# Kernel optimization log

Hardware: AMD Instinct MI355X
Metric: run time of the kernel (lower is better)

## Reference

```python
import jax, jax.numpy as jnp
import numpy as np

V, D, B, L = 433, 120, 4096, 16  # vocab, d_model, batch, seq_len
H4 = 4 * D
LN_EPS = 1e-5


def setup_inputs() -> dict:
    key = jax.random.key(0)
    ks = jax.random.split(key, 12)
    s = 1.0 / np.sqrt(D)  # PyTorch LSTM init range
    u = lambda k, shape: jax.random.uniform(k, shape, jnp.float32, -s, s)
    return {
        "x": jax.random.randint(ks[0], (B, L), 0, V, dtype=jnp.int32),
        "embed": jax.random.normal(ks[1], (V, D), jnp.float32) * 0.02,
        "Wih0": u(ks[2], (H4, D)), "Whh0": u(ks[3], (H4, D)),
        "bih0": u(ks[4], (H4,)), "bhh0": u(ks[5], (H4,)),
        "Wih1": u(ks[6], (H4, D)), "Whh1": u(ks[7], (H4, D)),
        "bih1": u(ks[8], (H4,)), "bhh1": u(ks[9], (H4,)),
        "gamma": jnp.ones((D,), jnp.float32),
        "beta": jnp.zeros((D,), jnp.float32),
    }


def _lstm_layer(x, Wih, Whh, bih, bhh):
    """One LSTM layer, batch_first input [B,L,D] -> [B,L,H]. PyTorch gate order i,f,g,o."""
    b, _, _ = x.shape
    h_dim = Whh.shape[1]
    # Precompute input contribution for all timesteps in one big GEMM.
    xg = jnp.einsum('bld,gd->blg', x, Wih) + bih + bhh  # [B,L,4H]

    def step(carry, g_t):
        h, c = carry
        gates = g_t + h @ Whh.T  # [B,4H]
        i, f, g, o = jnp.split(gates, 4, axis=-1)
        c = jax.nn.sigmoid(f) * c + jax.nn.sigmoid(i) * jnp.tanh(g)
        h = jax.nn.sigmoid(o) * jnp.tanh(c)
        return (h, c), h

    init = (jnp.zeros((b, h_dim), x.dtype), jnp.zeros((b, h_dim), x.dtype))
    _, hs = jax.lax.scan(step, init, jnp.swapaxes(xg, 0, 1))  # [L,B,H]
    return jnp.swapaxes(hs, 0, 1)


def _layernorm(h, gamma, beta):
    mu = jnp.mean(h, axis=-1, keepdims=True)
    var = jnp.mean(jnp.square(h - mu), axis=-1, keepdims=True)
    return (h - mu) / jnp.sqrt(var + LN_EPS) * gamma + beta


def reference(x, embed, Wih0, Whh0, bih0, bhh0, Wih1, Whh1, bih1, bhh1, gamma, beta):
    h = embed[x]                               # [B,L,D] token embedding
    h = _lstm_layer(h, Wih0, Whh0, bih0, bhh0)  # layer 0
    h = _lstm_layer(h, Wih1, Whh1, bih1, bhh1)  # layer 1
    out = _layernorm(h, gamma, beta)
    logits = jnp.einsum('bld,vd->blv', out, embed)  # tied-embedding head (no bias)
    return logits
```

## Files before the change

### kernel.cpp

```cpp
#include <hip/hip_runtime.h>


#define VSZ 433
#define DIM 120
#define BSZ 4096
#define SEQ 16
#define H4  480
#define KP  128
#define NPAD 448
#define NT_HEAD (NPAD/16)
#define TB  16
#define GP  484
#define HP  136

typedef unsigned int   u32;
typedef unsigned short u16;
typedef __attribute__((ext_vector_type(8))) short    v8bf;
typedef __attribute__((ext_vector_type(8))) _Float16 v8h;
typedef __attribute__((ext_vector_type(4))) float    v4f;

__device__ __forceinline__ u16 f2bf(float f){
  union{float f;u32 u;}z; z.f=f;
  u32 u = z.u + 0x7fffu + ((z.u>>16)&1u);
  return (u16)(u>>16);
}
__device__ __forceinline__ u32 packh2(float a, float b){
  union{_Float16 h[2]; u32 u;} z;
  z.h[0] = (_Float16)a; z.h[1] = (_Float16)b;
  return z.u;
}

#define EW_OFF   0u
#define B1S_OFF  831488u
#define EMBP_OFF 833408u
#define HB0_OFF  948096u

#define PREP_BLKS 113

__global__ __launch_bounds__(512) void k_init(const float* __restrict__ embed,
                                              const float* __restrict__ Wih0,
                                              const float* __restrict__ bih0,
                                              const float* __restrict__ bhh0,
                                              const float* __restrict__ bih1,
                                              const float* __restrict__ bhh1,
                                              float* __restrict__ EW,
                                              u16* __restrict__ embP,
                                              float* __restrict__ b1s)
{
  __shared__ float e[DIM];
  const int tid = threadIdx.x;
  if (blockIdx.x < VSZ) {
    const int v = blockIdx.x;
    if (tid < DIM) e[tid] = embed[v*DIM + tid];
    __syncthreads();
    if (tid < H4) {
      float acc = bih0[tid] + bhh0[tid];
      #pragma unroll
      for (int k0 = 0; k0 < DIM; k0 += 4) {
        float4 w = *(const float4*)(Wih0 + tid*DIM + k0);
        acc = fmaf(e[k0+0], w.x, acc);
        acc = fmaf(e[k0+1], w.y, acc);
        acc = fmaf(e[k0+2], w.z, acc);
        acc = fmaf(e[k0+3], w.w, acc);
      }
      EW[v*H4 + tid] = acc;
    }
  } else {
    const int idx = (blockIdx.x - VSZ)*512 + tid;
    if (idx < NPAD*KP) {
      int n = idx >> 7, k = idx & 127;
      embP[idx] = (n < VSZ && k < DIM) ? f2bf(embed[n*DIM + k]) : (u16)0;
    } else if (idx < NPAD*KP + H4) {
      int g = idx - NPAD*KP;
      b1s[g] = bih1[g] + bhh1[g];
    }
  }
}

__global__ __launch_bounds__(512) void k_rec(const float* __restrict__ Whh0,
                                             const float* __restrict__ EW,
                                             const int* __restrict__ x,
                                             const float* __restrict__ Wih1,
                                             const float* __restrict__ Whh1,
                                             const float* __restrict__ b1s,
                                             const float* __restrict__ gamma,
                                             const float* __restrict__ beta,
                                             const u16* __restrict__ embP,
                                             _Float16* __restrict__ hb0,
                                             float* __restrict__ out)
{
  __shared__ float gLs[TB][GP];
  __shared__ __align__(16) _Float16 hLh[TB][HP];
  __shared__ __align__(16) u16 hnL[TB][HP];
  __shared__ __align__(16) u16 embL[NPAD][HP];
  __shared__ int xL[TB*SEQ];

  const int tid  = threadIdx.x;
  const int wave = tid >> 6, lane = tid & 63;
  const int cl   = lane & 15, quad = lane >> 4;
  const int b0   = blockIdx.x * TB;

  for (int i = tid; i < TB*SEQ; i += 512) xL[i] = x[b0*SEQ + i];
  for (int i = tid; i < TB*HP; i += 512) (&hLh[0][0])[i] = (_Float16)0.f;
  for (int c = tid; c < NPAD*16; c += 512) {
    const int rw = c >> 4, c16 = c & 15;
    *(v8bf*)&embL[rw][c16*8] = *(const v8bf*)&embP[(size_t)rw*KP + c16*8];
  }
  __syncthreads();

  const int prow = wave*2;
  const bool act = lane < 60;
  const int d0   = lane*2;

  {
    v8h Bf[4][4];
    #pragma unroll
    for (int i = 0; i < 4; ++i) {
      const int nt = wave*4 + i;
      const bool vld = (nt < 30);
      const int n = vld ? nt*16 + cl : 0;
      #pragma unroll
      for (int kt = 0; kt < 4; ++kt) {
        const int k0 = kt*32 + quad*8;
        v8h f = {0,0,0,0,0,0,0,0};
        if (vld && k0 < DIM) {
          float4 q0 = *(const float4*)(Whh0 + n*DIM + k0);
          float4 q1 = *(const float4*)(Whh0 + n*DIM + k0 + 4);
          f[0]=(_Float16)q0.x; f[1]=(_Float16)q0.y; f[2]=(_Float16)q0.z; f[3]=(_Float16)q0.w;
          f[4]=(_Float16)q1.x; f[5]=(_Float16)q1.y; f[6]=(_Float16)q1.z; f[7]=(_Float16)q1.w;
        }
        Bf[i][kt] = f;
      }
    }

    float srcv[4][4];
    auto load_src = [&](int t) {
      #pragma unroll
      for (int i = 0; i < 4; ++i) {
        const int nt = wave*4 + i;
        if (nt < 30) {
          const int n = nt*16 + cl;
          #pragma unroll
          for (int r = 0; r < 4; ++r)
            srcv[i][r] = EW[(size_t)xL[(quad*4 + r)*SEQ + t]*H4 + n];
        }
      }
    };
    load_src(0);

    float C0[2][2] = {{0.f,0.f},{0.f,0.f}};

    for (int t = 0; t < SEQ; ++t) {
      __syncthreads();
      v8h Af[4];
      #pragma unroll
      for (int kt = 0; kt < 4; ++kt)
        Af[kt] = *(const v8h*)&hLh[cl][kt*32 + quad*8];
      v4f acc[4];
      #pragma unroll
      for (int i = 0; i < 4; ++i) {
        acc[i][0]=srcv[i][0]; acc[i][1]=srcv[i][1];
        acc[i][2]=srcv[i][2]; acc[i][3]=srcv[i][3];
      }
      #pragma unroll
      for (int i = 0; i < 4; ++i)
        if (wave*4 + i < 30) {
          #pragma unroll
          for (int kt = 0; kt < 4; ++kt)
            acc[i] = __builtin_amdgcn_mfma_f32_16x16x32_f16(Af[kt], Bf[i][kt], acc[i], 0, 0, 0);
        }
      if (t + 1 < SEQ) load_src(t + 1);
      #pragma unroll
      for (int i = 0; i < 4; ++i) {
        const int nt = wave*4 + i;
        if (nt < 30) {
          #pragma unroll
          for (int r = 0; r < 4; ++r)
            gLs[quad*4 + r][nt*16 + cl] = acc[i][r];
        }
      }
      __syncthreads();
      #pragma unroll
      for (int rr = 0; rr < 2; ++rr) {
        const int row = prow + rr;
        if (act) {
          const float2 gi = *(const float2*)&gLs[row][d0      ];
          const float2 gf = *(const float2*)&gLs[row][d0 + 120];
          const float2 gg = *(const float2*)&gLs[row][d0 + 240];
          const float2 go = *(const float2*)&gLs[row][d0 + 360];
          float h2[2];
          #pragma unroll
          for (int k = 0; k < 2; ++k) {
            const float vi = k ? gi.y : gi.x, vf = k ? gf.y : gf.x;
            const float vg = k ? gg.y : gg.x, vo = k ? go.y : go.x;
            const float si = 1.f / (1.f + __expf(-vi));
            const float sf = 1.f / (1.f + __expf(-vf));
            const float tg = 1.f - 2.f / (__expf(2.f*vg) + 1.f);
            const float so = 1.f / (1.f + __expf(-vo));
            const float c  = sf * C0[rr][k] + si * tg;
            C0[rr][k] = c;
            const float tc = 1.f - 2.f / (__expf(2.f*c) + 1.f);
            h2[k] = so * tc;
          }
          *(u32*)&hLh[row][d0] = packh2(h2[0], h2[1]);
          *(u32*)&hb0[((size_t)t*BSZ + b0 + row)*KP + d0] = packh2(h2[0], h2[1]);
        } else {
          *(u32*)&hb0[((size_t)t*BSZ + b0 + row)*KP + 120 + 2*(lane - 60)] = 0u;
        }
      }
    }
  }

  __syncthreads();

  const float* Wih1p = Wih1;
  const float* Whh1p = Whh1;
  const float* b1sp  = b1s;
  asm volatile("" : "+s"(Wih1p), "+s"(Whh1p), "+s"(b1sp) :: "memory");

  for (int i = tid; i < TB*HP; i += 512) (&hLh[0][0])[i] = (_Float16)0.f;

  v8h Bi[4][4], Bh[4][4];
  float bias[4];
  #pragma unroll
  for (int i = 0; i < 4; ++i) {
    const int nt = wave*4 + i;
    const bool vld = (nt < 30);
    const int n = vld ? nt*16 + cl : 0;
    bias[i] = vld ? b1sp[n] : 0.f;
    #pragma unroll
    for (int kt = 0; kt < 4; ++kt) {
      const int k0 = kt*32 + quad*8;
      v8h fi = {0,0,0,0,0,0,0,0}, fh = {0,0,0,0,0,0,0,0};
      if (vld && k0 < DIM) {
        float4 q0 = *(const float4*)(Wih1p + n*DIM + k0);
        float4 q1 = *(const float4*)(Wih1p + n*DIM + k0 + 4);
        fi[0]=(_Float16)q0.x; fi[1]=(_Float16)q0.y; fi[2]=(_Float16)q0.z; fi[3]=(_Float16)q0.w;
        fi[4]=(_Float16)q1.x; fi[5]=(_Float16)q1.y; fi[6]=(_Float16)q1.z; fi[7]=(_Float16)q1.w;
        float4 p0 = *(const float4*)(Whh1p + n*DIM + k0);
        float4 p1 = *(const float4*)(Whh1p + n*DIM + k0 + 4);
        fh[0]=(_Float16)p0.x; fh[1]=(_Float16)p0.y; fh[2]=(_Float16)p0.z; fh[3]=(_Float16)p0.w;
        fh[4]=(_Float16)p1.x; fh[5]=(_Float16)p1.y; fh[6]=(_Float16)p1.z; fh[7]=(_Float16)p1.w;
      }
      Bi[i][kt] = fi;
      Bh[i][kt] = fh;
    }
  }

  float gmm[2] = {0.f, 0.f}, bta[2] = {0.f, 0.f};
  if (act) {
    gmm[0] = gamma[d0]; gmm[1] = gamma[d0+1];
    bta[0] = beta[d0];  bta[1] = beta[d0+1];
  }
  float C1[2][2] = {{0.f,0.f},{0.f,0.f}};

  v8h A0n[4];
  #pragma unroll
  for (int kt = 0; kt < 4; ++kt)
    A0n[kt] = *(const v8h*)&hb0[((size_t)0*BSZ + b0 + cl)*KP + kt*32 + quad*8];
  __syncthreads();

  for (int t = 0; t < SEQ; ++t) {
    v8h A0c[4], A1[4];
    #pragma unroll
    for (int kt = 0; kt < 4; ++kt) A0c[kt] = A0n[kt];
    #pragma unroll
    for (int kt = 0; kt < 4; ++kt)
      A1[kt] = *(const v8h*)&hLh[cl][kt*32 + quad*8];
    if (t + 1 < SEQ) {
      #pragma unroll
      for (int kt = 0; kt < 4; ++kt)
        A0n[kt] = *(const v8h*)&hb0[((size_t)(t+1)*BSZ + b0 + cl)*KP + kt*32 + quad*8];
    }
    v4f acc[4];
    #pragma unroll
    for (int i = 0; i < 4; ++i)
      acc[i] = (v4f){bias[i], bias[i], bias[i], bias[i]};
    #pragma unroll
    for (int i = 0; i < 4; ++i)
      if (wave*4 + i < 30) {
        #pragma unroll
        for (int kt = 0; kt < 4; ++kt) {
          acc[i] = __builtin_amdgcn_mfma_f32_16x16x32_f16(A0c[kt], Bi[i][kt], acc[i], 0, 0, 0);
          acc[i] = __builtin_amdgcn_mfma_f32_16x16x32_f16(A1[kt],  Bh[i][kt], acc[i], 0, 0, 0);
        }
      }
    #pragma unroll
    for (int i = 0; i < 4; ++i) {
      const int nt = wave*4 + i;
      if (nt < 30) {
        #pragma unroll
        for (int r = 0; r < 4; ++r)
          gLs[quad*4 + r][nt*16 + cl] = acc[i][r];
      }
    }
    __syncthreads();
    float h2[2][2] = {{0.f,0.f},{0.f,0.f}};
    float s1[2] = {0.f, 0.f}, s2[2] = {0.f, 0.f};
    #pragma unroll
    for (int rr = 0; rr < 2; ++rr) {
      const int row = prow + rr;
      if (act) {
        const float2 gi = *(const float2*)&gLs[row][d0      ];
        const float2 gf = *(const float2*)&gLs[row][d0 + 120];
        const float2 gg = *(const float2*)&gLs[row][d0 + 240];
        const float2 go = *(const float2*)&gLs[row][d0 + 360];
        #pragma unroll
        for (int k = 0; k < 2; ++k) {
          const float vi = k ? gi.y : gi.x, vf = k ? gf.y : gf.x;
          const float vg = k ? gg.y : gg.x, vo = k ? go.y : go.x;
          const float si = 1.f / (1.f + __expf(-vi));
          const float sf = 1.f / (1.f + __expf(-vf));
          const float tg = 1.f - 2.f / (__expf(2.f*vg) + 1.f);
          const float so = 1.f / (1.f + __expf(-vo));
          const float c  = sf * C1[rr][k] + si * tg;
          C1[rr][k] = c;
          const float tc = 1.f - 2.f / (__expf(2.f*c) + 1.f);
          const float h  = so * tc;
          h2[rr][k] = h;
          s1[rr] += h;
          s2[rr] = fmaf(h, h, s2[rr]);
        }
        *(u32*)&hLh[row][d0] = packh2(h2[rr][0], h2[rr][1]);
      }
    }
    #pragma unroll
    for (int m = 32; m >= 1; m >>= 1) {
      s1[0] += __shfl_xor(s1[0], m);
      s2[0] += __shfl_xor(s2[0], m);
      s1[1] += __shfl_xor(s1[1], m);
      s2[1] += __shfl_xor(s2[1], m);
    }
    #pragma unroll
    for (int rr = 0; rr < 2; ++rr) {
      const int row = prow + rr;
      const float mu = s1[rr] * (1.f/DIM);
      const float var = s2[rr] * (1.f/DIM) - mu*mu;
      const float rs = rsqrtf(var + 1e-5f);
      if (act) {
        const float v0 = fmaf((h2[rr][0] - mu)*rs, gmm[0], bta[0]);
        const float v1 = fmaf((h2[rr][1] - mu)*rs, gmm[1], bta[1]);
        *(u32*)&hnL[row][d0] = (u32)f2bf(v0) | ((u32)f2bf(v1) << 16);
      } else {
        *(u32*)&hnL[row][120 + 2*(lane - 60)] = 0u;
      }
    }
    __syncthreads();

    {
      v8bf a[4];
      #pragma unroll
      for (int kt = 0; kt < 4; ++kt)
        a[kt] = *(const v8bf*)&hnL[cl][kt*32 + quad*8];
      #pragma unroll
      for (int j = 0; j < 4; ++j) {
        const int nt = wave + 8*j;
        if (nt < NT_HEAD) {
          const int n = nt*16 + cl;
          v8bf bfr[4];
          #pragma unroll
          for (int kt = 0; kt < 4; ++kt)
            bfr[kt] = *(const v8bf*)&embL[n][kt*32 + quad*8];
          v4f hacc = {0.f, 0.f, 0.f, 0.f};
          #pragma unroll
          for (int kt = 0; kt < 4; ++kt)
            hacc = __builtin_amdgcn_mfma_f32_16x16x32_bf16(a[kt], bfr[kt], hacc, 0, 0, 0);
          if (n < VSZ) {
            #pragma unroll
            for (int r = 0; r < 4; ++r)
              out[((size_t)(b0 + quad*4 + r)*SEQ + t)*VSZ + n] = hacc[r];
          }
        }
      }
    }
  }
}

extern "C" void kernel_launch(void* const* d_in, const int* in_sizes, int n_in,
                              void* d_out, int out_size, void* d_ws, size_t ws_size,
                              hipStream_t stream)
{
  (void)in_sizes; (void)n_in; (void)out_size; (void)ws_size;
  const int*   x     = (const int*)d_in[0];
  const float* embed = (const float*)d_in[1];
  const float* Wih0  = (const float*)d_in[2];
  const float* Whh0  = (const float*)d_in[3];
  const float* bih0  = (const float*)d_in[4];
  const float* bhh0  = (const float*)d_in[5];
  const float* Wih1  = (const float*)d_in[6];
  const float* Whh1  = (const float*)d_in[7];
  const float* bih1  = (const float*)d_in[8];
  const float* bhh1  = (const float*)d_in[9];
  const float* gamma = (const float*)d_in[10];
  const float* beta  = (const float*)d_in[11];

  char* ws = (char*)d_ws;
  float*     EW   = (float*)(ws + EW_OFF);
  float*     b1s  = (float*)(ws + B1S_OFF);
  u16*       embP = (u16*)(ws + EMBP_OFF);
  _Float16*  hb0  = (_Float16*)(ws + HB0_OFF);

  k_init<<<VSZ + PREP_BLKS, 512, 0, stream>>>(embed, Wih0, bih0, bhh0, bih1, bhh1,
                                              EW, embP, b1s);
  k_rec <<<BSZ/TB, 512, 0, stream>>>(Whh0, EW, x, Wih1, Whh1, b1s, gamma, beta,
                                     embP, hb0, (float*)d_out);
}
```

Measured before the change: 257.2 us.

## Interleave gate columns per wave, keep layer-0 states in LDS, pipeline head behind LSTM

Gate rows are permuted so that each wave's MFMA output tile holds the i,f,g,o values for its own hidden units. The cell update then reads from a per-wave scratch with only a wave barrier, which removes one block-wide barrier per step and the shared gate buffer. Layer-0 hidden states stay in LDS instead of round-tripping through global memory. The embedding head reads a pre-swizzled fragment layout straight from global memory instead of staging into LDS. Layer-1 recurrence, the LayerNorm reduction via a partial-sum buffer, and the head GEMM are software-pipelined across steps with double buffers. The cost is larger LDS use from the sixteen-step hb0 buffer and the head B operand coming through cache rather than LDS.

```diff
diff --git a/kernel.cpp b/kernel.cpp
--- a/kernel.cpp
+++ b/kernel.cpp
@@ -8,10 +8,10 @@
 #define H4  480
 #define KP  128
 #define NPAD 448
-#define NT_HEAD (NPAD/16)
+#define NT_HEAD 28
 #define TB  16
-#define GP  484
 #define HP  136
+#define SCRW 68
 
 typedef unsigned int   u32;
 typedef unsigned short u16;
@@ -30,12 +30,12 @@
   return z.u;
 }
 
-#define EW_OFF   0u
-#define B1S_OFF  831488u
-#define EMBP_OFF 833408u
-#define HB0_OFF  948096u
-
-#define PREP_BLKS 113
+#define EW_OFF    0u
+#define B1S_OFF   831488u
+#define EMBF_OFF  833408u
+
+#define PREP_N    (NPAD*KP + H4)
+#define PREP_BLKS ((PREP_N + 511)/512)
 
 __global__ __launch_bounds__(512) void k_init(const float* __restrict__ embed,
                                               const float* __restrict__ Wih0,
@@ -44,7 +44,7 @@
                                               const float* __restrict__ bih1,
                                               const float* __restrict__ bhh1,
                                               float* __restrict__ EW,
-                                              u16* __restrict__ embP,
+                                              u16* __restrict__ embF,
                                               float* __restrict__ b1s)
 {
   __shared__ float e[DIM];
@@ -69,8 +69,10 @@
     const int idx = (blockIdx.x - VSZ)*512 + tid;
     if (idx < NPAD*KP) {
       int n = idx >> 7, k = idx & 127;
-      embP[idx] = (n < VSZ && k < DIM) ? f2bf(embed[n*DIM + k]) : (u16)0;
-    } else if (idx < NPAD*KP + H4) {
+      int nt = n >> 4, cl = n & 15, kt = k >> 5, quad = (k >> 3) & 3, j = k & 7;
+      int fidx = ((((nt*4 + kt)*4 + quad)*16 + cl) << 3) + j;
+      embF[fidx] = (n < VSZ && k < DIM) ? f2bf(embed[n*DIM + k]) : (u16)0;
+    } else if (idx < PREP_N) {
       int g = idx - NPAD*KP;
       b1s[g] = bih1[g] + bhh1[g];
     }
@@ -85,160 +87,145 @@
                                              const float* __restrict__ b1s,
                                              const float* __restrict__ gamma,
                                              const float* __restrict__ beta,
-                                             const u16* __restrict__ embP,
-                                             _Float16* __restrict__ hb0,
+                                             const u16* __restrict__ embF,
                                              float* __restrict__ out)
 {
-  __shared__ float gLs[TB][GP];
-  __shared__ __align__(16) _Float16 hLh[TB][HP];
-  __shared__ __align__(16) u16 hnL[TB][HP];
-  __shared__ __align__(16) u16 embL[NPAD][HP];
+  __shared__ float scr[8][TB][SCRW];
+  __shared__ __align__(16) _Float16 hLh0[2][TB][HP];
+  __shared__ __align__(16) _Float16 hLh1[2][TB][HP];
+  __shared__ __align__(16) u16 hnLD[2][TB][HP];
+  __shared__ __align__(16) _Float16 hb0L[SEQ][TB][HP];
+  __shared__ float prt[2][TB][8][2];
   __shared__ int xL[TB*SEQ];
 
   const int tid  = threadIdx.x;
   const int wave = tid >> 6, lane = tid & 63;
   const int cl   = lane & 15, quad = lane >> 4;
   const int b0   = blockIdx.x * TB;
+  const int row  = lane & 15, lg = lane >> 4;
+  const int dl0  = wave*16 + lg*4;
+  const bool vdim = (dl0 < DIM);
 
   for (int i = tid; i < TB*SEQ; i += 512) xL[i] = x[b0*SEQ + i];
-  for (int i = tid; i < TB*HP; i += 512) (&hLh[0][0])[i] = (_Float16)0.f;
-  for (int c = tid; c < NPAD*16; c += 512) {
-    const int rw = c >> 4, c16 = c & 15;
-    *(v8bf*)&embL[rw][c16*8] = *(const v8bf*)&embP[(size_t)rw*KP + c16*8];
-  }
+  for (int i = tid; i < 2*TB*HP; i += 512) {
+    (&hLh0[0][0][0])[i] = (_Float16)0.f;
+    (&hLh1[0][0][0])[i] = (_Float16)0.f;
+  }
+
+  int orow[4];
+  #pragma unroll
+  for (int i = 0; i < 4; ++i) {
+    const int p = (wave*4 + i)*16 + cl;
+    orow[i] = (p & 3)*120 + (p >> 2);
+  }
+
+  v8h Bf0[4][4];
+  #pragma unroll
+  for (int i = 0; i < 4; ++i) {
+    const bool vld = (wave*4 + i < 30);
+    #pragma unroll
+    for (int kt = 0; kt < 4; ++kt) {
+      const int k0 = kt*32 + quad*8;
+      v8h f = {0,0,0,0,0,0,0,0};
+      if (vld && k0 < DIM) {
+        float4 q0 = *(const float4*)(Whh0 + orow[i]*DIM + k0);
+        float4 q1 = *(const float4*)(Whh0 + orow[i]*DIM + k0 + 4);
+        f[0]=(_Float16)q0.x; f[1]=(_Float16)q0.y; f[2]=(_Float16)q0.z; f[3]=(_Float16)q0.w;
+        f[4]=(_Float16)q1.x; f[5]=(_Float16)q1.y; f[6]=(_Float16)q1.z; f[7]=(_Float16)q1.w;
+      }
+      Bf0[i][kt] = f;
+    }
+  }
+
+  float srcv[4][4] = {{0.f,0.f,0.f,0.f},{0.f,0.f,0.f,0.f},
+                      {0.f,0.f,0.f,0.f},{0.f,0.f,0.f,0.f}};
+  auto load_src = [&](int t) {
+    #pragma unroll
+    for (int i = 0; i < 4; ++i) {
+      if (wave*4 + i < 30) {
+        #pragma unroll
+        for (int r = 0; r < 4; ++r)
+          srcv[i][r] = EW[(size_t)xL[(quad*4 + r)*SEQ + t]*H4 + orow[i]];
+      }
+    }
+  };
   __syncthreads();
-
-  const int prow = wave*2;
-  const bool act = lane < 60;
-  const int d0   = lane*2;
-
-  {
-    v8h Bf[4][4];
+  load_src(0);
+
+  float C0[4] = {0.f, 0.f, 0.f, 0.f};
+
+  for (int t = 0; t < SEQ; ++t) {
+    v8h Af[4];
+    #pragma unroll
+    for (int kt = 0; kt < 4; ++kt)
+      Af[kt] = *(const v8h*)&hLh0[t & 1][cl][kt*32 + quad*8];
+    v4f acc[4];
     #pragma unroll
     for (int i = 0; i < 4; ++i) {
-      const int nt = wave*4 + i;
-      const bool vld = (nt < 30);
-      const int n = vld ? nt*16 + cl : 0;
-      #pragma unroll
-      for (int kt = 0; kt < 4; ++kt) {
-        const int k0 = kt*32 + quad*8;
-        v8h f = {0,0,0,0,0,0,0,0};
-        if (vld && k0 < DIM) {
-          float4 q0 = *(const float4*)(Whh0 + n*DIM + k0);
-          float4 q1 = *(const float4*)(Whh0 + n*DIM + k0 + 4);
-          f[0]=(_Float16)q0.x; f[1]=(_Float16)q0.y; f[2]=(_Float16)q0.z; f[3]=(_Float16)q0.w;
-          f[4]=(_Float16)q1.x; f[5]=(_Float16)q1.y; f[6]=(_Float16)q1.z; f[7]=(_Float16)q1.w;
-        }
-        Bf[i][kt] = f;
-      }
-    }
-
-    float srcv[4][4];
-    auto load_src = [&](int t) {
-      #pragma unroll
-      for (int i = 0; i < 4; ++i) {
-        const int nt = wave*4 + i;
-        if (nt < 30) {
-          const int n = nt*16 + cl;
-          #pragma unroll
-          for (int r = 0; r < 4; ++r)
-            srcv[i][r] = EW[(size_t)xL[(quad*4 + r)*SEQ + t]*H4 + n];
-        }
-      }
-    };
-    load_src(0);
-
-    float C0[2][2] = {{0.f,0.f},{0.f,0.f}};
-
-    for (int t = 0; t < SEQ; ++t) {
-      __syncthreads();
-      v8h Af[4];
-      #pragma unroll
-      for (int kt = 0; kt < 4; ++kt)
-        Af[kt] = *(const v8h*)&hLh[cl][kt*32 + quad*8];
-      v4f acc[4];
-      #pragma unroll
-      for (int i = 0; i < 4; ++i) {
-        acc[i][0]=srcv[i][0]; acc[i][1]=srcv[i][1];
-        acc[i][2]=srcv[i][2]; acc[i][3]=srcv[i][3];
-      }
+      acc[i][0]=srcv[i][0]; acc[i][1]=srcv[i][1];
+      acc[i][2]=srcv[i][2]; acc[i][3]=srcv[i][3];
+    }
+    #pragma unroll
+    for (int kt = 0; kt < 4; ++kt)
       #pragma unroll
       for (int i = 0; i < 4; ++i)
-        if (wave*4 + i < 30) {
-          #pragma unroll
-          for (int kt = 0; kt < 4; ++kt)
-            acc[i] = __builtin_amdgcn_mfma_f32_16x16x32_f16(Af[kt], Bf[i][kt], acc[i], 0, 0, 0);
-        }
-      if (t + 1 < SEQ) load_src(t + 1);
-      #pragma unroll
-      for (int i = 0; i < 4; ++i) {
-        const int nt = wave*4 + i;
-        if (nt < 30) {
-          #pragma unroll
-          for (int r = 0; r < 4; ++r)
-            gLs[quad*4 + r][nt*16 + cl] = acc[i][r];
-        }
-      }
-      __syncthreads();
-      #pragma unroll
-      for (int rr = 0; rr < 2; ++rr) {
-        const int row = prow + rr;
-        if (act) {
-          const float2 gi = *(const float2*)&gLs[row][d0      ];
-          const float2 gf = *(const float2*)&gLs[row][d0 + 120];
-          const float2 gg = *(const float2*)&gLs[row][d0 + 240];
-          const float2 go = *(const float2*)&gLs[row][d0 + 360];
-          float h2[2];
-          #pragma unroll
-          for (int k = 0; k < 2; ++k) {
-            const float vi = k ? gi.y : gi.x, vf = k ? gf.y : gf.x;
-            const float vg = k ? gg.y : gg.x, vo = k ? go.y : go.x;
-            const float si = 1.f / (1.f + __expf(-vi));
-            const float sf = 1.f / (1.f + __expf(-vf));
-            const float tg = 1.f - 2.f / (__expf(2.f*vg) + 1.f);
-            const float so = 1.f / (1.f + __expf(-vo));
-            const float c  = sf * C0[rr][k] + si * tg;
-            C0[rr][k] = c;
-            const float tc = 1.f - 2.f / (__expf(2.f*c) + 1.f);
-            h2[k] = so * tc;
-          }
-          *(u32*)&hLh[row][d0] = packh2(h2[0], h2[1]);
-          *(u32*)&hb0[((size_t)t*BSZ + b0 + row)*KP + d0] = packh2(h2[0], h2[1]);
-        } else {
-          *(u32*)&hb0[((size_t)t*BSZ + b0 + row)*KP + 120 + 2*(lane - 60)] = 0u;
-        }
-      }
-    }
-  }
-
-  __syncthreads();
+        if (wave*4 + i < 30)
+          acc[i] = __builtin_amdgcn_mfma_f32_16x16x32_f16(Af[kt], Bf0[i][kt], acc[i], 0, 0, 0);
+    if (t + 1 < SEQ) load_src(t + 1);
+    #pragma unroll
+    for (int i = 0; i < 4; ++i)
+      if (wave*4 + i < 30) {
+        #pragma unroll
+        for (int r = 0; r < 4; ++r)
+          scr[wave][quad*4 + r][16*i + cl] = acc[i][r];
+      }
+    __builtin_amdgcn_wave_barrier();
+    asm volatile("s_waitcnt lgkmcnt(0)" ::: "memory");
+    __builtin_amdgcn_sched_barrier(0);
+    float h0v[4];
+    #pragma unroll
+    for (int j = 0; j < 4; ++j) {
+      const float4 gq = *(const float4*)&scr[wave][row][16*lg + 4*j];
+      const float si = 1.f / (1.f + __expf(-gq.x));
+      const float sf = 1.f / (1.f + __expf(-gq.y));
+      const float tg = 1.f - 2.f / (__expf(2.f*gq.z) + 1.f);
+      const float so = 1.f / (1.f + __expf(-gq.w));
+      const float c  = sf * C0[j] + si * tg;
+      C0[j] = c;
+      const float tc = 1.f - 2.f / (__expf(2.f*c) + 1.f);
+      h0v[j] = so * tc;
+    }
+    uint2 pk; pk.x = 0u; pk.y = 0u;
+    if (vdim) { pk.x = packh2(h0v[0], h0v[1]); pk.y = packh2(h0v[2], h0v[3]); }
+    *(uint2*)&hLh0[(t+1) & 1][row][dl0] = pk;
+    *(uint2*)&hb0L[t][row][dl0] = pk;
+    __syncthreads();
+  }
 
   const float* Wih1p = Wih1;
   const float* Whh1p = Whh1;
   const float* b1sp  = b1s;
-  asm volatile("" : "+s"(Wih1p), "+s"(Whh1p), "+s"(b1sp) :: "memory");
-
-  for (int i = tid; i < TB*HP; i += 512) (&hLh[0][0])[i] = (_Float16)0.f;
+  const float* gmp   = gamma;
+  const float* btp   = beta;
+  asm volatile("" : "+s"(Wih1p), "+s"(Whh1p), "+s"(b1sp), "+s"(gmp), "+s"(btp) :: "memory");
 
   v8h Bi[4][4], Bh[4][4];
   float bias[4];
   #pragma unroll
   for (int i = 0; i < 4; ++i) {
-    const int nt = wave*4 + i;
-    const bool vld = (nt < 30);
-    const int n = vld ? nt*16 + cl : 0;
-    bias[i] = vld ? b1sp[n] : 0.f;
+    const bool vld = (wave*4 + i < 30);
+    bias[i] = vld ? b1sp[orow[i]] : 0.f;
     #pragma unroll
     for (int kt = 0; kt < 4; ++kt) {
       const int k0 = kt*32 + quad*8;
       v8h fi = {0,0,0,0,0,0,0,0}, fh = {0,0,0,0,0,0,0,0};
       if (vld && k0 < DIM) {
-        float4 q0 = *(const float4*)(Wih1p + n*DIM + k0);
-        float4 q1 = *(const float4*)(Wih1p + n*DIM + k0 + 4);
+        float4 q0 = *(const float4*)(Wih1p + orow[i]*DIM + k0);
+        float4 q1 = *(const float4*)(Wih1p + orow[i]*DIM + k0 + 4);
         fi[0]=(_Float16)q0.x; fi[1]=(_Float16)q0.y; fi[2]=(_Float16)q0.z; fi[3]=(_Float16)q0.w;
         fi[4]=(_Float16)q1.x; fi[5]=(_Float16)q1.y; fi[6]=(_Float16)q1.z; fi[7]=(_Float16)q1.w;
-        float4 p0 = *(const float4*)(Whh1p + n*DIM + k0);
-        float4 p1 = *(const float4*)(Whh1p + n*DIM + k0 + 4);
+        float4 p0 = *(const float4*)(Whh1p + orow[i]*DIM + k0);
+        float4 p1 = *(const float4*)(Whh1p + orow[i]*DIM + k0 + 4);
         fh[0]=(_Float16)p0.x; fh[1]=(_Float16)p0.y; fh[2]=(_Float16)p0.z; fh[3]=(_Float16)p0.w;
         fh[4]=(_Float16)p1.x; fh[5]=(_Float16)p1.y; fh[6]=(_Float16)p1.z; fh[7]=(_Float16)p1.w;
       }
@@ -246,125 +233,56 @@
       Bh[i][kt] = fh;
     }
   }
-
-  float gmm[2] = {0.f, 0.f}, bta[2] = {0.f, 0.f};
-  if (act) {
-    gmm[0] = gamma[d0]; gmm[1] = gamma[d0+1];
-    bta[0] = beta[d0];  bta[1] = beta[d0+1];
-  }
-  float C1[2][2] = {{0.f,0.f},{0.f,0.f}};
-
-  v8h A0n[4];
-  #pragma unroll
-  for (int kt = 0; kt < 4; ++kt)
-    A0n[kt] = *(const v8h*)&hb0[((size_t)0*BSZ + b0 + cl)*KP + kt*32 + quad*8];
-  __syncthreads();
-
-  for (int t = 0; t < SEQ; ++t) {
-    v8h A0c[4], A1[4];
-    #pragma unroll
-    for (int kt = 0; kt < 4; ++kt) A0c[kt] = A0n[kt];
-    #pragma unroll
-    for (int kt = 0; kt < 4; ++kt)
-      A1[kt] = *(const v8h*)&hLh[cl][kt*32 + quad*8];
-    if (t + 1 < SEQ) {
+  float gmm4[4] = {0.f,0.f,0.f,0.f}, bta4[4] = {0.f,0.f,0.f,0.f};
+  if (vdim) {
+    #pragma unroll
+    for (int j = 0; j < 4; ++j) { gmm4[j] = gmp[dl0+j]; bta4[j] = btp[dl0+j]; }
+  }
+  float C1[4] = {0.f,0.f,0.f,0.f};
+  float h1prev[4] = {0.f,0.f,0.f,0.f};
+
+  for (int s = 0; s <= SEQ + 1; ++s) {
+    if (s >= 1 && s <= SEQ) {
+      const float* pr = &prt[(s-1) & 1][row][0][0];
+      const float4 q0 = *(const float4*)(pr);
+      const float4 q1 = *(const float4*)(pr + 4);
+      const float4 q2 = *(const float4*)(pr + 8);
+      const float4 q3 = *(const float4*)(pr + 12);
+      const float s1 = q0.x+q0.z + q1.x+q1.z + q2.x+q2.z + q3.x+q3.z;
+      const float s2 = q0.y+q0.w + q1.y+q1.w + q2.y+q2.w + q3.y+q3.w;
+      const float mu = s1 * (1.f/DIM);
+      const float var = s2 * (1.f/DIM) - mu*mu;
+      const float rs = rsqrtf(var + 1e-5f);
+      uint2 pk; pk.x = 0u; pk.y = 0u;
+      if (vdim) {
+        const float v0 = fmaf((h1prev[0]-mu)*rs, gmm4[0], bta4[0]);
+        const float v1 = fmaf((h1prev[1]-mu)*rs, gmm4[1], bta4[1]);
+        const float v2 = fmaf((h1prev[2]-mu)*rs, gmm4[2], bta4[2]);
+        const float v3 = fmaf((h1prev[3]-mu)*rs, gmm4[3], bta4[3]);
+        pk.x = (u32)f2bf(v0) | ((u32)f2bf(v1) << 16);
+        pk.y = (u32)f2bf(v2) | ((u32)f2bf(v3) << 16);
+      }
+      *(uint2*)&hnLD[(s-1) & 1][row][dl0] = pk;
+    }
+    if (s >= 2) {
+      const int t = s - 2;
+      v8bf a[4];
       #pragma unroll
       for (int kt = 0; kt < 4; ++kt)
-        A0n[kt] = *(const v8h*)&hb0[((size_t)(t+1)*BSZ + b0 + cl)*KP + kt*32 + quad*8];
-    }
-    v4f acc[4];
-    #pragma unroll
-    for (int i = 0; i < 4; ++i)
-      acc[i] = (v4f){bias[i], bias[i], bias[i], bias[i]};
-    #pragma unroll
-    for (int i = 0; i < 4; ++i)
-      if (wave*4 + i < 30) {
-        #pragma unroll
-        for (int kt = 0; kt < 4; ++kt) {
-          acc[i] = __builtin_amdgcn_mfma_f32_16x16x32_f16(A0c[kt], Bi[i][kt], acc[i], 0, 0, 0);
-          acc[i] = __builtin_amdgcn_mfma_f32_16x16x32_f16(A1[kt],  Bh[i][kt], acc[i], 0, 0, 0);
-        }
-      }
-    #pragma unroll
-    for (int i = 0; i < 4; ++i) {
-      const int nt = wave*4 + i;
-      if (nt < 30) {
-        #pragma unroll
-        for (int r = 0; r < 4; ++r)
-          gLs[quad*4 + r][nt*16 + cl] = acc[i][r];
-      }
-    }
-    __syncthreads();
-    float h2[2][2] = {{0.f,0.f},{0.f,0.f}};
-    float s1[2] = {0.f, 0.f}, s2[2] = {0.f, 0.f};
-    #pragma unroll
-    for (int rr = 0; rr < 2; ++rr) {
-      const int row = prow + rr;
-      if (act) {
-        const float2 gi = *(const float2*)&gLs[row][d0      ];
-        const float2 gf = *(const float2*)&gLs[row][d0 + 120];
-        const float2 gg = *(const float2*)&gLs[row][d0 + 240];
-        const float2 go = *(const float2*)&gLs[row][d0 + 360];
-        #pragma unroll
-        for (int k = 0; k < 2; ++k) {
-          const float vi = k ? gi.y : gi.x, vf = k ? gf.y : gf.x;
-          const float vg = k ? gg.y : gg.x, vo = k ? go.y : go.x;
-          const float si = 1.f / (1.f + __expf(-vi));
-          const float sf = 1.f / (1.f + __expf(-vf));
-          const float tg = 1.f - 2.f / (__expf(2.f*vg) + 1.f);
-          const float so = 1.f / (1.f + __expf(-vo));
-          const float c  = sf * C1[rr][k] + si * tg;
-          C1[rr][k] = c;
-          const float tc = 1.f - 2.f / (__expf(2.f*c) + 1.f);
-          const float h  = so * tc;
-          h2[rr][k] = h;
-          s1[rr] += h;
-          s2[rr] = fmaf(h, h, s2[rr]);
-        }
-        *(u32*)&hLh[row][d0] = packh2(h2[rr][0], h2[rr][1]);
-      }
-    }
-    #pragma unroll
-    for (int m = 32; m >= 1; m >>= 1) {
-      s1[0] += __shfl_xor(s1[0], m);
-      s2[0] += __shfl_xor(s2[0], m);
-      s1[1] += __shfl_xor(s1[1], m);
-      s2[1] += __shfl_xor(s2[1], m);
-    }
-    #pragma unroll
-    for (int rr = 0; rr < 2; ++rr) {
-      const int row = prow + rr;
-      const float mu = s1[rr] * (1.f/DIM);
-      const float var = s2[rr] * (1.f/DIM) - mu*mu;
-      const float rs = rsqrtf(var + 1e-5f);
-      if (act) {
-        const float v0 = fmaf((h2[rr][0] - mu)*rs, gmm[0], bta[0]);
-        const float v1 = fmaf((h2[rr][1] - mu)*rs, gmm[1], bta[1]);
-        *(u32*)&hnL[row][d0] = (u32)f2bf(v0) | ((u32)f2bf(v1) << 16);
-      } else {
-        *(u32*)&hnL[row][120 + 2*(lane - 60)] = 0u;
-      }
-    }
-    __syncthreads();
-
-    {
-      v8bf a[4];
-      #pragma unroll
-      for (int kt = 0; kt < 4; ++kt)
-        a[kt] = *(const v8bf*)&hnL[cl][kt*32 + quad*8];
+        a[kt] = *(const v8bf*)&hnLD[(s-2) & 1][cl][kt*32 + quad*8];
       #pragma unroll
       for (int j = 0; j < 4; ++j) {
-        const int nt = wave + 8*j;
-        if (nt < NT_HEAD) {
-          const int n = nt*16 + cl;
+        const int nth = wave + 8*j;
+        if (nth < NT_HEAD) {
           v8bf bfr[4];
           #pragma unroll
           for (int kt = 0; kt < 4; ++kt)
-            bfr[kt] = *(const v8bf*)&embL[n][kt*32 + quad*8];
+            bfr[kt] = *(const v8bf*)&embF[(((size_t)nth*4 + kt)*64 + lane)*8];
           v4f hacc = {0.f, 0.f, 0.f, 0.f};
           #pragma unroll
           for (int kt = 0; kt < 4; ++kt)
             hacc = __builtin_amdgcn_mfma_f32_16x16x32_bf16(a[kt], bfr[kt], hacc, 0, 0, 0);
+          const int n = nth*16 + cl;
           if (n < VSZ) {
             #pragma unroll
             for (int r = 0; r < 4; ++r)
@@ -373,6 +291,64 @@
         }
       }
     }
+    if (s < SEQ) {
+      v8h A0[4], A1[4];
+      #pragma unroll
+      for (int kt = 0; kt < 4; ++kt) {
+        A0[kt] = *(const v8h*)&hb0L[s][cl][kt*32 + quad*8];
+        A1[kt] = *(const v8h*)&hLh1[s & 1][cl][kt*32 + quad*8];
+      }
+      v4f acc[4];
+      #pragma unroll
+      for (int i = 0; i < 4; ++i)
+        acc[i] = (v4f){bias[i], bias[i], bias[i], bias[i]};
+      #pragma unroll
+      for (int kt = 0; kt < 4; ++kt)
+        #pragma unroll
+        for (int i = 0; i < 4; ++i)
+          if (wave*4 + i < 30) {
+            acc[i] = __builtin_amdgcn_mfma_f32_16x16x32_f16(A0[kt], Bi[i][kt], acc[i], 0, 0, 0);
+            acc[i] = __builtin_amdgcn_mfma_f32_16x16x32_f16(A1[kt], Bh[i][kt], acc[i], 0, 0, 0);
+          }
+      #pragma unroll
+      for (int i = 0; i < 4; ++i)
+        if (wave*4 + i < 30) {
+          #pragma unroll
+          for (int r = 0; r < 4; ++r)
+            scr[wave][quad*4 + r][16*i + cl] = acc[i][r];
+        }
+      __builtin_amdgcn_wave_barrier();
+      asm volatile("s_waitcnt lgkmcnt(0)" ::: "memory");
+      __builtin_amdgcn_sched_barrier(0);
+      #pragma unroll
+      for (int j = 0; j < 4; ++j) {
+        const float4 gq = *(const float4*)&scr[wave][row][16*lg + 4*j];
+        const float si = 1.f / (1.f + __expf(-gq.x));
+        const float sf = 1.f / (1.f + __expf(-gq.y));
+        const float tg = 1.f - 2.f / (__expf(2.f*gq.z) + 1.f);
+        const float so = 1.f / (1.f + __expf(-gq.w));
+        const float c  = sf * C1[j] + si * tg;
+        C1[j] = c;
+        const float tc = 1.f - 2.f / (__expf(2.f*c) + 1.f);
+        h1prev[j] = so * tc;
+      }
+      uint2 pk; pk.x = 0u; pk.y = 0u;
+      if (vdim) { pk.x = packh2(h1prev[0], h1prev[1]); pk.y = packh2(h1prev[2], h1prev[3]); }
+      *(uint2*)&hLh1[(s+1) & 1][row][dl0] = pk;
+      float s1l = 0.f, s2l = 0.f;
+      if (vdim) {
+        s1l = h1prev[0] + h1prev[1] + h1prev[2] + h1prev[3];
+        s2l = h1prev[0]*h1prev[0] + h1prev[1]*h1prev[1]
+            + h1prev[2]*h1prev[2] + h1prev[3]*h1prev[3];
+      }
+      s1l += __shfl_xor(s1l, 16); s1l += __shfl_xor(s1l, 32);
+      s2l += __shfl_xor(s2l, 16); s2l += __shfl_xor(s2l, 32);
+      if (lane < 16) {
+        prt[s & 1][lane][wave][0] = s1l;
+        prt[s & 1][lane][wave][1] = s2l;
+      }
+    }
+    __syncthreads();
   }
 }
 
@@ -395,13 +371,12 @@
   const float* beta  = (const float*)d_in[11];
 
   char* ws = (char*)d_ws;
-  float*     EW   = (float*)(ws + EW_OFF);
-  float*     b1s  = (float*)(ws + B1S_OFF);
-  u16*       embP = (u16*)(ws + EMBP_OFF);
-  _Float16*  hb0  = (_Float16*)(ws + HB0_OFF);
+  float* EW   = (float*)(ws + EW_OFF);
+  float* b1s  = (float*)(ws + B1S_OFF);
+  u16*   embF = (u16*)(ws + EMBF_OFF);
 
   k_init<<<VSZ + PREP_BLKS, 512, 0, stream>>>(embed, Wih0, bih0, bhh0, bih1, bhh1,
-                                              EW, embP, b1s);
+                                              EW, embF, b1s);
   k_rec <<<BSZ/TB, 512, 0, stream>>>(Whh0, EW, x, Wih1, Whh1, b1s, gamma, beta,
-                                     embP, hb0, (float*)d_out);
-}
+                                     embF, (float*)d_out);
+}
```

Result: slower. 320.3 us (+24.5%).

## Keep layer-0 hidden states in LDS and read head weights pre-swizzled from global

Applied to the files above, without the earlier changes.

Layer-0 hidden states for all timesteps now stay in a shared-memory buffer instead of a global scratch array that layer 1 read back. The 448x136 bf16 embedding copy in LDS is removed. The head GEMM now loads its B fragments straight from a global buffer that k_init writes in MFMA fragment order, so each lane reads contiguous 16-byte chunks. NT_HEAD drops to 28, which skips the all-padding tile. Together these cut LDS use, which may allow more blocks per CU, and remove a global round trip, at the cost of head weights being read from L2/global on every timestep.

```diff
diff --git a/kernel.cpp b/kernel.cpp
--- a/kernel.cpp
+++ b/kernel.cpp
@@ -8,7 +8,7 @@
 #define H4  480
 #define KP  128
 #define NPAD 448
-#define NT_HEAD (NPAD/16)
+#define NT_HEAD 28
 #define TB  16
 #define GP  484
 #define HP  136
@@ -30,12 +30,12 @@
   return z.u;
 }
 
-#define EW_OFF   0u
-#define B1S_OFF  831488u
-#define EMBP_OFF 833408u
-#define HB0_OFF  948096u
-
-#define PREP_BLKS 113
+#define EW_OFF    0u
+#define B1S_OFF   831488u
+#define EMBF_OFF  833408u
+
+#define PREP_N    (NPAD*KP + H4)
+#define PREP_BLKS ((PREP_N + 511)/512)
 
 __global__ __launch_bounds__(512) void k_init(const float* __restrict__ embed,
                                               const float* __restrict__ Wih0,
@@ -44,7 +44,7 @@
                                               const float* __restrict__ bih1,
                                               const float* __restrict__ bhh1,
                                               float* __restrict__ EW,
-                                              u16* __restrict__ embP,
+                                              u16* __restrict__ embF,
                                               float* __restrict__ b1s)
 {
   __shared__ float e[DIM];
@@ -69,8 +69,10 @@
     const int idx = (blockIdx.x - VSZ)*512 + tid;
     if (idx < NPAD*KP) {
       int n = idx >> 7, k = idx & 127;
-      embP[idx] = (n < VSZ && k < DIM) ? f2bf(embed[n*DIM + k]) : (u16)0;
-    } else if (idx < NPAD*KP + H4) {
+      int nt = n >> 4, cl = n & 15, kt = k >> 5, quad = (k >> 3) & 3, j = k & 7;
+      int fidx = ((((nt*4 + kt)*4 + quad)*16 + cl) << 3) + j;
+      embF[fidx] = (n < VSZ && k < DIM) ? f2bf(embed[n*DIM + k]) : (u16)0;
+    } else if (idx < PREP_N) {
       int g = idx - NPAD*KP;
       b1s[g] = bih1[g] + bhh1[g];
     }
@@ -85,14 +87,13 @@
                                              const float* __restrict__ b1s,
                                              const float* __restrict__ gamma,
                                              const float* __restrict__ beta,
-                                             const u16* __restrict__ embP,
-                                             _Float16* __restrict__ hb0,
+                                             const u16* __restrict__ embF,
                                              float* __restrict__ out)
 {
   __shared__ float gLs[TB][GP];
+  __shared__ __align__(16) _Float16 hb0L[SEQ+1][TB][HP];
   __shared__ __align__(16) _Float16 hLh[TB][HP];
   __shared__ __align__(16) u16 hnL[TB][HP];
-  __shared__ __align__(16) u16 embL[NPAD][HP];
   __shared__ int xL[TB*SEQ];
 
   const int tid  = threadIdx.x;
@@ -101,10 +102,10 @@
   const int b0   = blockIdx.x * TB;
 
   for (int i = tid; i < TB*SEQ; i += 512) xL[i] = x[b0*SEQ + i];
-  for (int i = tid; i < TB*HP; i += 512) (&hLh[0][0])[i] = (_Float16)0.f;
-  for (int c = tid; c < NPAD*16; c += 512) {
-    const int rw = c >> 4, c16 = c & 15;
-    *(v8bf*)&embL[rw][c16*8] = *(const v8bf*)&embP[(size_t)rw*KP + c16*8];
+  {
+    u32* p = (u32*)&hb0L[0][0][0];
+    for (int i = tid; i < (SEQ+1)*TB*HP/2; i += 512) p[i] = 0u;
+    for (int i = tid; i < TB*HP; i += 512) (&hLh[0][0])[i] = (_Float16)0.f;
   }
   __syncthreads();
 
@@ -133,7 +134,8 @@
       }
     }
 
-    float srcv[4][4];
+    float srcv[4][4] = {{0.f,0.f,0.f,0.f},{0.f,0.f,0.f,0.f},
+                        {0.f,0.f,0.f,0.f},{0.f,0.f,0.f,0.f}};
     auto load_src = [&](int t) {
       #pragma unroll
       for (int i = 0; i < 4; ++i) {
@@ -155,7 +157,7 @@
       v8h Af[4];
       #pragma unroll
       for (int kt = 0; kt < 4; ++kt)
-        Af[kt] = *(const v8h*)&hLh[cl][kt*32 + quad*8];
+        Af[kt] = *(const v8h*)&hb0L[t][cl][kt*32 + quad*8];
       v4f acc[4];
       #pragma unroll
       for (int i = 0; i < 4; ++i) {
@@ -202,10 +204,7 @@
             const float tc = 1.f - 2.f / (__expf(2.f*c) + 1.f);
             h2[k] = so * tc;
           }
-          *(u32*)&hLh[row][d0] = packh2(h2[0], h2[1]);
-          *(u32*)&hb0[((size_t)t*BSZ + b0 + row)*KP + d0] = packh2(h2[0], h2[1]);
-        } else {
-          *(u32*)&hb0[((size_t)t*BSZ + b0 + row)*KP + 120 + 2*(lane - 60)] = 0u;
+          *(u32*)&hb0L[t+1][row][d0] = packh2(h2[0], h2[1]);
         }
       }
     }
@@ -217,8 +216,6 @@
   const float* Whh1p = Whh1;
   const float* b1sp  = b1s;
   asm volatile("" : "+s"(Wih1p), "+s"(Whh1p), "+s"(b1sp) :: "memory");
-
-  for (int i = tid; i < TB*HP; i += 512) (&hLh[0][0])[i] = (_Float16)0.f;
 
   v8h Bi[4][4], Bh[4][4];
   float bias[4];
@@ -253,24 +250,14 @@
     bta[0] = beta[d0];  bta[1] = beta[d0+1];
   }
   float C1[2][2] = {{0.f,0.f},{0.f,0.f}};
-
-  v8h A0n[4];
-  #pragma unroll
-  for (int kt = 0; kt < 4; ++kt)
-    A0n[kt] = *(const v8h*)&hb0[((size_t)0*BSZ + b0 + cl)*KP + kt*32 + quad*8];
   __syncthreads();
 
   for (int t = 0; t < SEQ; ++t) {
     v8h A0c[4], A1[4];
     #pragma unroll
-    for (int kt = 0; kt < 4; ++kt) A0c[kt] = A0n[kt];
-    #pragma unroll
-    for (int kt = 0; kt < 4; ++kt)
-      A1[kt] = *(const v8h*)&hLh[cl][kt*32 + quad*8];
-    if (t + 1 < SEQ) {
-      #pragma unroll
-      for (int kt = 0; kt < 4; ++kt)
-        A0n[kt] = *(const v8h*)&hb0[((size_t)(t+1)*BSZ + b0 + cl)*KP + kt*32 + quad*8];
+    for (int kt = 0; kt < 4; ++kt) {
+      A0c[kt] = *(const v8h*)&hb0L[t+1][cl][kt*32 + quad*8];
+      A1[kt]  = *(const v8h*)&hLh[cl][kt*32 + quad*8];
     }
     v4f acc[4];
     #pragma unroll
@@ -356,15 +343,15 @@
       for (int j = 0; j < 4; ++j) {
         const int nt = wave + 8*j;
         if (nt < NT_HEAD) {
-          const int n = nt*16 + cl;
           v8bf bfr[4];
           #pragma unroll
           for (int kt = 0; kt < 4; ++kt)
-            bfr[kt] = *(const v8bf*)&embL[n][kt*32 + quad*8];
+            bfr[kt] = *(const v8bf*)&embF[(((size_t)nt*4 + kt)*64 + lane)*8];
           v4f hacc = {0.f, 0.f, 0.f, 0.f};
           #pragma unroll
           for (int kt = 0; kt < 4; ++kt)
             hacc = __builtin_amdgcn_mfma_f32_16x16x32_bf16(a[kt], bfr[kt], hacc, 0, 0, 0);
+          const int n = nt*16 + cl;
           if (n < VSZ) {
             #pragma unroll
             for (int r = 0; r < 4; ++r)
@@ -395,13 +382,12 @@
   const float* beta  = (const float*)d_in[11];
 
   char* ws = (char*)d_ws;
-  float*     EW   = (float*)(ws + EW_OFF);
-  float*     b1s  = (float*)(ws + B1S_OFF);
-  u16*       embP = (u16*)(ws + EMBP_OFF);
-  _Float16*  hb0  = (_Float16*)(ws + HB0_OFF);
+  float* EW   = (float*)(ws + EW_OFF);
+  float* b1s  = (float*)(ws + B1S_OFF);
+  u16*   embF = (u16*)(ws + EMBF_OFF);
 
   k_init<<<VSZ + PREP_BLKS, 512, 0, stream>>>(embed, Wih0, bih0, bhh0, bih1, bhh1,
-                                              EW, embP, b1s);
+                                              EW, embF, b1s);
   k_rec <<<BSZ/TB, 512, 0, stream>>>(Whh0, EW, x, Wih1, Whh1, b1s, gamma, beta,
-                                     embP, hb0, (float*)d_out);
-}
+                                     embF, (float*)d_out);
+}
```

Result: slower. 263.7 us (+2.5%).
